# Kernel tuning notes

Measured on AMD Instinct MI355X. Metric: run time of the kernel, lower is better.

Reference implementation:

```python
import jax, jax.numpy as jnp
import numpy as np

N_ROI = 262144
FEATURE_DIM = 256
HIDDEN_DIM = 64
N_NETWORKS = 128


def setup_inputs() -> dict:
    key = jax.random.key(0)
    ks = jax.random.split(key, 5)
    x = jax.random.normal(ks[0], (N_ROI, FEATURE_DIM), dtype=jnp.float32)
    group = jax.random.randint(ks[1], (N_ROI,), 0, N_NETWORKS, dtype=jnp.int32)
    W1 = jax.random.normal(ks[2], (FEATURE_DIM, HIDDEN_DIM), dtype=jnp.float32) / np.sqrt(FEATURE_DIM)
    b1 = jnp.zeros((HIDDEN_DIM,), dtype=jnp.float32)
    W2 = jax.random.normal(ks[3], (HIDDEN_DIM, 1), dtype=jnp.float32) / np.sqrt(HIDDEN_DIM)
    b2 = jnp.zeros((1,), dtype=jnp.float32)
    return {"x": x, "group": group, "W1": W1, "b1": b1, "W2": W2, "b2": b2}


def reference(x, group, W1, b1, W2, b2):
    # attention MLP score per ROI: Linear -> ReLU -> Linear(->1)
    h = jax.nn.relu(x @ W1 + b1)                       # [N, H]
    score = (h @ W2)[:, 0] + b2[0]                     # [N]
    # numerically-stable segment softmax over each network's ROIs
    seg_max = jax.ops.segment_max(score, group, num_segments=N_NETWORKS)  # [K]
    seg_max = jnp.where(jnp.isfinite(seg_max), seg_max, 0.0)              # empty segments -> 0
    w = jnp.exp(score - seg_max[group])                # [N] unnormalized weights
    denom = jax.ops.segment_sum(w, group, num_segments=N_NETWORKS)        # [K]
    num = jax.ops.segment_sum(w[:, None] * x, group, num_segments=N_NETWORKS)  # [K, D]
    # empty networks produce zeros (matches torch.zeros_like branch)
    return jnp.where(denom[:, None] > 0, num / jnp.maximum(denom, 1e-30)[:, None], 0.0)
```

## Files before the change

### kernel.cpp

```cpp
#include <hip/hip_runtime.h>
#include <hip/hip_bf16.h>

#define N_ROI 262144
#define FDIM  256
#define HDIM  64
#define NNET  128

#define CHUNK  64
#define NCHUNK 16
#define RPB    (CHUNK * NCHUNK)
#define NBLK   (N_ROI / RPB)
#define XPITCH 264
#define WPITCH 264
#define APITCH 72
#define STRIP  40.0f

typedef __attribute__((ext_vector_type(8))) __bf16 bf16x8;
typedef __attribute__((ext_vector_type(8))) short short8;
typedef __attribute__((ext_vector_type(4))) float floatx4;

union frag_cast { short8 s; bf16x8 b; };

#define NEG_INF (-__builtin_huge_valf())

__device__ __forceinline__ unsigned fkey(float f) {
  unsigned u = __float_as_uint(f);
  return (u & 0x80000000u) ? ~u : (u | 0x80000000u);
}
__device__ __forceinline__ float fkey_inv(unsigned k) {
  unsigned u = (k & 0x80000000u) ? (k ^ 0x80000000u) : ~k;
  return __uint_as_float(u);
}
__device__ __forceinline__ unsigned short f2bf(float f) {
  unsigned u = __float_as_uint(f);
  u += 0x7FFFu + ((u >> 16) & 1u);
  return (unsigned short)(u >> 16);
}
__device__ __forceinline__ float bf2f(unsigned short h) {
  return __uint_as_float(((unsigned)h) << 16);
}
__device__ __forceinline__ unsigned cvt2(float a, float b) {
  union { __hip_bfloat162 h; unsigned u; } cv;
  cv.h = __float22bfloat162_rn(make_float2(a, b));
  return cv.u;
}
__device__ __forceinline__ int sidx(int row, int s) {
  return row * XPITCH + (s ^ (((row >> 3) & 3) << 4));
}

__device__ __forceinline__ void block_bar() {
  __builtin_amdgcn_sched_barrier(0);
  asm volatile("s_waitcnt lgkmcnt(0)");
  __builtin_amdgcn_s_barrier();
  __builtin_amdgcn_sched_barrier(0);
}

__global__ __launch_bounds__(1024, 4) void fused_kernel(
    const float* __restrict__ x, const int* __restrict__ group,
    const float* __restrict__ W1, const float* __restrict__ b1,
    const float* __restrict__ W2,
    float* __restrict__ num_ws,
    float* __restrict__ den_ws,
    float* __restrict__ m_ws)
{
  __shared__ __align__(16) unsigned short w1t[HDIM][WPITCH];
  __shared__ __align__(16) unsigned short xl[2][CHUNK * XPITCH];
  __shared__ __align__(16) unsigned short Alds[NNET * APITCH];
  __shared__ float scpart[4][CHUNK];
  __shared__ unsigned tmax[NNET];
  __shared__ __align__(16) float fl[NNET];
  __shared__ float mrunL[NNET];
  __shared__ float dent[NNET];
  __shared__ int sflag;

  const int tid  = threadIdx.x;
  const int wave = tid >> 6, lane = tid & 63;
  const int col  = lane & 15, quad = lane >> 4;
  const int h    = wave >> 2;
  const int mt   = wave & 3;
  const int bid  = blockIdx.x;
  const size_t rbase = (size_t)bid * RPB;

  {
    const int n = tid & 63, kg = tid >> 6;
#pragma unroll
    for (int p = 0; p < 2; ++p) {
      const int k0 = (p * 16 + kg) * 8;
      unsigned short tmp[8];
#pragma unroll
      for (int j = 0; j < 8; ++j) tmp[j] = f2bf(W1[(k0 + j) * HDIM + n]);
      *(short8*)&w1t[n][k0] = *(short8*)tmp;
    }
  }
  if (tid < NNET) mrunL[tid] = 0.f;
  float denrun = 0.f;

  const float b1s = b1[h * 16 + col];
  const float w2s = W2[h * 16 + col];

  floatx4 acc[8];
#pragma unroll
  for (int m2 = 0; m2 < 8; ++m2) acc[m2] = (floatx4)0.f;

  const float* xb = x + rbase * FDIM;
  const short8 zero8 = (short8)0;

  float4 pf[4];
#pragma unroll
  for (int i = 0; i < 4; ++i) pf[i] = *(const float4*)(xb + i * 4096 + tid * 4);
#pragma unroll
  for (int i = 0; i < 4; ++i) {
    const int row = i * 16 + wave;
    uint2 pk; pk.x = cvt2(pf[i].x, pf[i].y); pk.y = cvt2(pf[i].z, pf[i].w);
    *(uint2*)&xl[0][sidx(row, (tid & 63) * 4)] = pk;
  }
#pragma unroll
  for (int i = 0; i < 4; ++i)
    pf[i] = *(const float4*)(xb + 16384 + i * 4096 + tid * 4);
  block_bar();

  for (int ch = 0; ch < NCHUNK; ++ch) {
    const int b = ch & 1;

    int gch = 0;
    if (tid < CHUNK) gch = group[rbase + ch * CHUNK + tid];

    for (int k8 = tid; k8 < (NNET * APITCH) / 8; k8 += 1024)
      *(short8*)&Alds[k8 * 8] = zero8;
    if (tid < NNET) dent[tid] = 0.f;
    if (tid == 0) sflag = 0;

    floatx4 accS = (floatx4)0.f;
#pragma unroll
    for (int c = 0; c < 8; ++c) {
      frag_cast af, bw;
      af.s = *(const short8*)&xl[b][sidx(mt * 16 + col, c * 32 + quad * 8)];
      bw.s = *(const short8*)&w1t[h * 16 + col][c * 32 + quad * 8];
      accS = __builtin_amdgcn_mfma_f32_16x16x32_bf16(af.b, bw.b, accS, 0, 0, 0);
    }
    {
      float pr[4];
#pragma unroll
      for (int r = 0; r < 4; ++r) pr[r] = fmaxf(accS[r] + b1s, 0.f) * w2s;
#pragma unroll
      for (int off = 1; off < 16; off <<= 1)
#pragma unroll
        for (int r = 0; r < 4; ++r) pr[r] += __shfl_xor(pr[r], off, 16);
      if (col == 0) {
#pragma unroll
        for (int r = 0; r < 4; ++r) scpart[h][mt * 16 + quad * 4 + r] = pr[r];
      }
    }
    block_bar();

    if (tid < CHUNK) {
      const float s = scpart[0][tid] + scpart[1][tid] + scpart[2][tid] + scpart[3][tid];
      scpart[0][tid] = s;
      const float m = mrunL[gch];
      const bool trip = !(s - m <= STRIP);
      const unsigned long long bal = __ballot(trip);
      if (bal == 0ull) {
        const float w = __expf(s - m);
        const unsigned short wb = f2bf(w);
        Alds[gch * APITCH + tid] = wb;
        atomicAdd(&dent[gch], bf2f(wb));
      } else if (tid == 0) {
        sflag = 1;
      }
    }
    if (ch < NCHUNK - 1) {
#pragma unroll
      for (int i = 0; i < 4; ++i) {
        const int row = i * 16 + wave;
        uint2 pk; pk.x = cvt2(pf[i].x, pf[i].y); pk.y = cvt2(pf[i].z, pf[i].w);
        *(uint2*)&xl[b ^ 1][sidx(row, (tid & 63) * 4)] = pk;
      }
      if (ch < NCHUNK - 2) {
#pragma unroll
        for (int i = 0; i < 4; ++i)
          pf[i] = *(const float4*)(xb + (size_t)(ch + 2) * 16384 + i * 4096 + tid * 4);
      }
    }
    block_bar();

    if (sflag) {
      if (tid < NNET) tmax[tid] = 0u;
      block_bar();
      if (tid < CHUNK) atomicMax(&tmax[gch], fkey(scpart[0][tid]));
      block_bar();
      if (tid < NNET) {
        const unsigned tk = tmax[tid];
        float f = 1.f;
        if (tk) {
          const float mn = fmaxf(mrunL[tid], fkey_inv(tk));
          f = __expf(mrunL[tid] - mn);
          mrunL[tid] = mn;
        }
        fl[tid] = f;
      }
      block_bar();
#pragma unroll
      for (int m2 = 0; m2 < 8; ++m2) {
        const floatx4 f4 = *(const floatx4*)&fl[m2 * 16 + quad * 4];
#pragma unroll
        for (int r = 0; r < 4; ++r) acc[m2][r] *= f4[r];
      }
      if (tid < NNET) denrun *= fl[tid];
      if (tid < CHUNK) {
        const float w = __expf(scpart[0][tid] - mrunL[gch]);
        const unsigned short wb = f2bf(w);
        Alds[gch * APITCH + tid] = wb;
        atomicAdd(&dent[gch], bf2f(wb));
      }
      block_bar();
    }

#pragma unroll
    for (int cc = 0; cc < 2; ++cc) {
      frag_cast bfx;
      {
        unsigned short bb[8];
#pragma unroll
        for (int j = 0; j < 8; ++j)
          bb[j] = xl[b][sidx(cc * 32 + quad * 8 + j, wave * 16 + col)];
        bfx.s = *(short8*)bb;
      }
#pragma unroll
      for (int m2 = 0; m2 < 8; ++m2) {
        frag_cast af;
        af.s = *(const short8*)&Alds[(m2 * 16 + col) * APITCH + cc * 32 + quad * 8];
        acc[m2] = __builtin_amdgcn_mfma_f32_16x16x32_bf16(af.b, bfx.b, acc[m2], 0, 0, 0);
      }
    }
    if (tid < NNET) denrun += dent[tid];
    block_bar();
  }

#pragma unroll
  for (int m2 = 0; m2 < 8; ++m2)
#pragma unroll
    for (int r = 0; r < 4; ++r) {
      const int g = m2 * 16 + quad * 4 + r;
      num_ws[((size_t)g * NBLK + bid) * FDIM + wave * 16 + col] = acc[m2][r];
    }
  if (tid < NNET) {
    den_ws[(size_t)tid * NBLK + bid] = denrun;
    m_ws[(size_t)tid * NBLK + bid]   = mrunL[tid];
  }
}

__global__ __launch_bounds__(256) void finalize_kernel(
    const float* __restrict__ num_ws, const float* __restrict__ den_ws,
    const float* __restrict__ m_ws, float* __restrict__ out)
{
  const int g   = blockIdx.x;
  const int tid = threadIdx.x;
  __shared__ float e_l[NBLK];
  __shared__ float red[8];

  const float mb = m_ws[(size_t)g * NBLK + tid];
  float M = mb;
#pragma unroll
  for (int off = 1; off < 64; off <<= 1) M = fmaxf(M, __shfl_xor(M, off));
  if ((tid & 63) == 0) red[tid >> 6] = M;
  __syncthreads();
  M = fmaxf(fmaxf(red[0], red[1]), fmaxf(red[2], red[3]));

  const float eb = (mb == NEG_INF) ? 0.f : __expf(mb - M);
  e_l[tid] = eb;
  float dp = den_ws[(size_t)g * NBLK + tid] * eb;
#pragma unroll
  for (int off = 1; off < 64; off <<= 1) dp += __shfl_xor(dp, off);
  if ((tid & 63) == 0) red[4 + (tid >> 6)] = dp;
  __syncthreads();
  const float den = red[4] + red[5] + red[6] + red[7];

  float nsum = 0.f;
  const float* base = num_ws + (size_t)g * NBLK * FDIM + tid;
#pragma unroll 8
  for (int b = 0; b < NBLK; ++b)
    nsum += base[(size_t)b * FDIM] * e_l[b];
  out[g * FDIM + tid] = (den > 0.f) ? nsum / fmaxf(den, 1e-30f) : 0.f;
}

extern "C" void kernel_launch(void* const* d_in, const int* in_sizes, int n_in,
                              void* d_out, int out_size, void* d_ws, size_t ws_size,
                              hipStream_t stream)
{
  const float* x     = (const float*)d_in[0];
  const int*   group = (const int*)d_in[1];
  const float* W1    = (const float*)d_in[2];
  const float* b1    = (const float*)d_in[3];
  const float* W2    = (const float*)d_in[4];
  float* out = (float*)d_out;

  float* num_ws = (float*)d_ws;
  float* den_ws = num_ws + (size_t)NNET * NBLK * FDIM;
  float* m_ws   = den_ws + (size_t)NNET * NBLK;

  fused_kernel<<<NBLK, 1024, 0, stream>>>(x, group, W1, b1, W2, num_ws, den_ws, m_ws);
  finalize_kernel<<<NNET, 256, 0, stream>>>(num_ws, den_ws, m_ws, out);

  (void)in_sizes; (void)n_in; (void)out_size; (void)ws_size;
}
```

Measured before the change: 384.0 us.

## Software-pipeline weighted-sum MFMA one chunk behind and drop extra barriers

```diff
diff --git a/kernel.cpp b/kernel.cpp
--- a/kernel.cpp
+++ b/kernel.cpp
@@ -50,7 +50,7 @@
 
 __device__ __forceinline__ void block_bar() {
   __builtin_amdgcn_sched_barrier(0);
-  asm volatile("s_waitcnt lgkmcnt(0)");
+  asm volatile("s_waitcnt lgkmcnt(0)" ::: "memory");
   __builtin_amdgcn_s_barrier();
   __builtin_amdgcn_sched_barrier(0);
 }
@@ -65,13 +65,13 @@
 {
   __shared__ __align__(16) unsigned short w1t[HDIM][WPITCH];
   __shared__ __align__(16) unsigned short xl[2][CHUNK * XPITCH];
-  __shared__ __align__(16) unsigned short Alds[NNET * APITCH];
+  __shared__ __align__(16) unsigned short Alds[2][NNET * APITCH];
   __shared__ float scpart[4][CHUNK];
   __shared__ unsigned tmax[NNET];
   __shared__ __align__(16) float fl[NNET];
   __shared__ float mrunL[NNET];
-  __shared__ float dent[NNET];
-  __shared__ int sflag;
+  __shared__ float dent[2][NNET];
+  __shared__ int sflag[2];
 
   const int tid  = threadIdx.x;
   const int wave = tid >> 6, lane = tid & 63;
@@ -92,7 +92,8 @@
       *(short8*)&w1t[n][k0] = *(short8*)tmp;
     }
   }
-  if (tid < NNET) mrunL[tid] = 0.f;
+  if (tid < NNET) { mrunL[tid] = 0.f; dent[1][tid] = 0.f; }
+  if (tid == 0) sflag[1] = 0;
   float denrun = 0.f;
 
   const float b1s = b1[h * 16 + col];
@@ -119,16 +120,26 @@
     pf[i] = *(const float4*)(xb + 16384 + i * 4096 + tid * 4);
   block_bar();
 
+  int gch = 0;
   for (int ch = 0; ch < NCHUNK; ++ch) {
     const int b = ch & 1;
 
-    int gch = 0;
+    if (sflag[b ^ 1]) {
+#pragma unroll
+      for (int m2 = 0; m2 < 8; ++m2) {
+        const floatx4 f4 = *(const floatx4*)&fl[m2 * 16 + quad * 4];
+#pragma unroll
+        for (int r = 0; r < 4; ++r) acc[m2][r] *= f4[r];
+      }
+      if (tid < NNET) denrun *= fl[tid];
+    }
+    if (tid < NNET) denrun += dent[b ^ 1][tid];
+
     if (tid < CHUNK) gch = group[rbase + ch * CHUNK + tid];
-
     for (int k8 = tid; k8 < (NNET * APITCH) / 8; k8 += 1024)
-      *(short8*)&Alds[k8 * 8] = zero8;
-    if (tid < NNET) dent[tid] = 0.f;
-    if (tid == 0) sflag = 0;
+      *(short8*)&Alds[b][k8 * 8] = zero8;
+    if (tid < NNET) { tmax[tid] = 0u; dent[b][tid] = 0.f; }
+    if (tid == 0) sflag[b] = 0;
 
     floatx4 accS = (floatx4)0.f;
 #pragma unroll
@@ -151,21 +162,63 @@
         for (int r = 0; r < 4; ++r) scpart[h][mt * 16 + quad * 4 + r] = pr[r];
       }
     }
+
+    if (ch > 0) {
+#pragma unroll
+      for (int cc = 0; cc < 2; ++cc) {
+        frag_cast bfx;
+        {
+          unsigned short bb[8];
+#pragma unroll
+          for (int j = 0; j < 8; ++j)
+            bb[j] = xl[b ^ 1][sidx(cc * 32 + quad * 8 + j, wave * 16 + col)];
+          bfx.s = *(short8*)bb;
+        }
+#pragma unroll
+        for (int m2 = 0; m2 < 8; ++m2) {
+          frag_cast af;
+          af.s = *(const short8*)&Alds[b ^ 1][(m2 * 16 + col) * APITCH + cc * 32 + quad * 8];
+          acc[m2] = __builtin_amdgcn_mfma_f32_16x16x32_bf16(af.b, bfx.b, acc[m2], 0, 0, 0);
+        }
+      }
+    }
     block_bar();
 
     if (tid < CHUNK) {
       const float s = scpart[0][tid] + scpart[1][tid] + scpart[2][tid] + scpart[3][tid];
-      scpart[0][tid] = s;
       const float m = mrunL[gch];
       const bool trip = !(s - m <= STRIP);
       const unsigned long long bal = __ballot(trip);
       if (bal == 0ull) {
         const float w = __expf(s - m);
         const unsigned short wb = f2bf(w);
-        Alds[gch * APITCH + tid] = wb;
-        atomicAdd(&dent[gch], bf2f(wb));
-      } else if (tid == 0) {
-        sflag = 1;
+        Alds[b][gch * APITCH + tid] = wb;
+        atomicAdd(&dent[b][gch], bf2f(wb));
+      } else {
+        atomicMax(&tmax[gch], fkey(s));
+        asm volatile("s_waitcnt lgkmcnt(0)" ::: "memory");
+#pragma unroll
+        for (int hh = 0; hh < 2; ++hh) {
+          const int gi = tid + hh * 64;
+          const unsigned tk = tmax[gi];
+          float f = 1.f;
+          float mo = mrunL[gi];
+          if (tk) {
+            const float mn = fmaxf(mo, fkey_inv(tk));
+            f = __expf(mo - mn);
+            mo = mn;
+            mrunL[gi] = mn;
+          }
+          fl[gi] = f;
+        }
+        asm volatile("s_waitcnt lgkmcnt(0)" ::: "memory");
+        {
+          const float w = __expf(s - mrunL[gch]);
+          const unsigned short wb = f2bf(w);
+          Alds[b][gch * APITCH + tid] = wb;
+          atomicAdd(&dent[b][gch], bf2f(wb));
+        }
+        if (tid == 0) sflag[b] = 1;
       }
     }
     if (ch < NCHUNK - 1) {
@@ -182,23 +235,11 @@
       }
     }
     block_bar();
-
-    if (sflag) {
-      if (tid < NNET) tmax[tid] = 0u;
-      block_bar();
-      if (tid < CHUNK) atomicMax(&tmax[gch], fkey(scpart[0][tid]));
-      block_bar();
-      if (tid < NNET) {
-        const unsigned tk = tmax[tid];
-        float f = 1.f;
-        if (tk) {
-          const float mn = fmaxf(mrunL[tid], fkey_inv(tk));
-          f = __expf(mrunL[tid] - mn);
-          mrunL[tid] = mn;
-        }
-        fl[tid] = f;
-      }
-      block_bar();
+  }
+
+  {
+    const int b = (NCHUNK - 1) & 1;
+    if (sflag[b]) {
 #pragma unroll
       for (int m2 = 0; m2 < 8; ++m2) {
         const floatx4 f4 = *(const floatx4*)&fl[m2 * 16 + quad * 4];
@@ -206,15 +247,8 @@
         for (int r = 0; r < 4; ++r) acc[m2][r] *= f4[r];
       }
       if (tid < NNET) denrun *= fl[tid];
-      if (tid < CHUNK) {
-        const float w = __expf(scpart[0][tid] - mrunL[gch]);
-        const unsigned short wb = f2bf(w);
-        Alds[gch * APITCH + tid] = wb;
-        atomicAdd(&dent[gch], bf2f(wb));
-      }
-      block_bar();
-    }
-
+    }
+    if (tid < NNET) denrun += dent[b][tid];
 #pragma unroll
     for (int cc = 0; cc < 2; ++cc) {
       frag_cast bfx;
@@ -228,12 +262,10 @@
 #pragma unroll
       for (int m2 = 0; m2 < 8; ++m2) {
         frag_cast af;
-        af.s = *(const short8*)&Alds[(m2 * 16 + col) * APITCH + cc * 32 + quad * 8];
+        af.s = *(const short8*)&Alds[b][(m2 * 16 + col) * APITCH + cc * 32 + quad * 8];
         acc[m2] = __builtin_amdgcn_mfma_f32_16x16x32_bf16(af.b, bfx.b, acc[m2], 0, 0, 0);
       }
     }
-    if (tid < NNET) denrun += dent[tid];
-    block_bar();
   }
 
 #pragma unroll
```

New measurement: 380.9 us. Within noise of the previous version (-0.8%).
